# Performance work log

Hardware: AMD Instinct MI355X
Metric: run time of the kernel (lower is better)

The kernel has to match this reference:

```python
import jax, jax.numpy as jnp
import numpy as np

N_HEADS = 8
HEAD_DIM = 64  # hidden_dim 512 / 8 heads
EPS = 1e-12    # F.normalize clamp_min eps


def setup_inputs() -> dict:
    key = jax.random.key(0)
    k1, k2, k3, k4 = jax.random.split(key, 4)
    B, C, H, W = 2, 256, 48, 48
    hidden = N_HEADS * HEAD_DIM
    x = jax.random.normal(k1, (B, C, H, W), dtype=jnp.float32)
    w_qkv = jax.random.normal(k2, (hidden * 3, C), dtype=jnp.float32) * 0.02
    w_proj = jax.random.normal(k3, (C, hidden), dtype=jnp.float32) * 0.02
    b_proj = jax.random.normal(k4, (C,), dtype=jnp.float32) * 0.02
    return {"x": x, "w_qkv": w_qkv, "w_proj": w_proj, "b_proj": b_proj}


def _l2norm_tokens(t):
    # normalize along the token axis (last dim), matching F.normalize(dim=-1)
    n = jnp.sqrt(jnp.sum(t * t, axis=-1, keepdims=True))
    return t / jnp.maximum(n, EPS)


def reference(x, w_qkv, w_proj, b_proj):
    B, C, H, W = x.shape
    N = H * W
    # 1x1 conv == channel matmul
    qkv = jnp.einsum('oc,bchw->bohw', w_qkv, x)  # [B, 3*hidden, H, W]
    qkv = qkv.reshape(B, 3, N_HEADS, HEAD_DIM, N)
    q, k, v = qkv[:, 0], qkv[:, 1], qkv[:, 2]    # each [B, h, d, N]
    q = _l2norm_tokens(q)
    k = _l2norm_tokens(k)
    # attn = q^T @ k over head_dim -> [B, h, N, N]; note: qk_scale unused in source
    attn = jnp.einsum('bhdn,bhdm->bhnm', q, k)
    attn = jax.nn.softmax(attn, axis=-1)
    # out = attn @ v^T -> [B, h, N, d], then permute to [B, h, d, N]
    out = jnp.einsum('bhnm,bhdm->bhdn', attn, v)
    out = out.reshape(B, N_HEADS * HEAD_DIM, H, W)
    # proj 1x1 conv with bias
    y = jnp.einsum('oc,bchw->bohw', w_proj, out) + b_proj[None, :, None, None]
    return y
```

## Files before the change

kernel.cpp:

```cpp
#include <hip/hip_runtime.h>
#include <math.h>

#define NTOK 2304
#define BATCH 2
#define CIN 256
#define HID 512
#define NH 8
#define LOG2E 1.44269504088896340736f

typedef __attribute__((ext_vector_type(8))) short bfrag;
typedef __attribute__((ext_vector_type(16))) float f32x16;

#if __has_builtin(__builtin_amdgcn_exp2f)
#define EXP2(x) __builtin_amdgcn_exp2f(x)
#else
#define EXP2(x) exp2f(x)
#endif

__device__ __forceinline__ unsigned f2bf(float f) {
    unsigned u = __float_as_uint(f);
    u += 0x7FFF + ((u >> 16) & 1);
    return u >> 16;
}

__device__ __forceinline__ float bf2f(unsigned short s) {
    return __uint_as_float(((unsigned)s) << 16);
}

__device__ __forceinline__ unsigned pk_trunc(float a, float b) {
    return __builtin_amdgcn_perm(__float_as_uint(b), __float_as_uint(a), 0x07060302u);
}

__device__ __forceinline__ void softmax_frag(
    const f32x16& accS, int h, float& ps0, float& ps1, bfrag& P0, bfrag& P1)
{
    unsigned dw[8];
    float e0[8], e1[8];
#pragma unroll
    for (int i = 0; i < 8; i++) {
        float plo = EXP2(accS[2 * i]);
        float phi = EXP2(accS[2 * i + 1]);
        dw[i] = pk_trunc(plo, phi);
        e0[i] = __uint_as_float(dw[i] << 16);
        e1[i] = __uint_as_float(dw[i] & 0xffff0000u);
    }
    ps0 += ((e0[0] + e0[1]) + (e0[2] + e0[3])) + ((e0[4] + e0[5]) + (e0[6] + e0[7]));
    ps1 += ((e1[0] + e1[1]) + (e1[2] + e1[3])) + ((e1[4] + e1[5]) + (e1[6] + e1[7]));
    unsigned sa0 = h ? dw[0] : dw[2], sb0 = h ? dw[1] : dw[3];
    unsigned sa1 = h ? dw[4] : dw[6], sb1 = h ? dw[5] : dw[7];
    unsigned ra0 = (unsigned)__shfl_xor((int)sa0, 32, 64);
    unsigned rb0 = (unsigned)__shfl_xor((int)sb0, 32, 64);
    unsigned ra1 = (unsigned)__shfl_xor((int)sa1, 32, 64);
    unsigned rb1 = (unsigned)__shfl_xor((int)sb1, 32, 64);
    union { bfrag f; unsigned u[4]; } U0, U1;
    U0.u[0] = h ? ra0 : dw[0];  U0.u[1] = h ? rb0 : dw[1];
    U0.u[2] = h ? dw[2] : ra0;  U0.u[3] = h ? dw[3] : rb0;
    U1.u[0] = h ? ra1 : dw[4];  U1.u[1] = h ? rb1 : dw[5];
    U1.u[2] = h ? dw[6] : ra1;  U1.u[3] = h ? dw[7] : rb1;
    P0 = U0.f; P1 = U1.f;
}

__global__ __launch_bounds__(256) void pack_all(
    const float* __restrict__ wq, short* __restrict__ wqb,
    const float* __restrict__ wp, short* __restrict__ wpb,
    const float* __restrict__ x, short* __restrict__ xT,
    float* __restrict__ sumsq)
{
    int bid = blockIdx.x;
    if (bid < 288) {
        int n0 = (bid % 36) * 64, c0 = ((bid / 36) & 3) * 64, b = bid / 144;
        __shared__ float sT[64][65];
        int tid = threadIdx.x, lane = tid & 63, wv = tid >> 6;
        for (int c = wv; c < 64; c += 4)
            sT[c][lane] = x[((size_t)b * CIN + c0 + c) * NTOK + n0 + lane];
        __syncthreads();
        int n = tid >> 2, c4 = (tid & 3) * 16;
        unsigned buf[8];
#pragma unroll
        for (int i = 0; i < 8; i++)
            buf[i] = f2bf(sT[c4 + 2 * i][n]) | (f2bf(sT[c4 + 2 * i + 1][n]) << 16);
        int n_tok = n0 + n;
        int l31n = n & 31;
        short* dst = xT + (((size_t)b * 72 + (n_tok >> 5)) * 16 + ((c0 + c4) >> 4)) * 512;
        ((uint4*)(dst + (0 * 32 + l31n) * 8))[0] = make_uint4(buf[0], buf[1], buf[2], buf[3]);
        ((uint4*)(dst + (1 * 32 + l31n) * 8))[0] = make_uint4(buf[4], buf[5], buf[6], buf[7]);
    } else {
        if (bid == 288) {
            ((float4*)sumsq)[threadIdx.x * 2] = make_float4(0.f, 0.f, 0.f, 0.f);
            ((float4*)sumsq)[threadIdx.x * 2 + 1] = make_float4(0.f, 0.f, 0.f, 0.f);
        }
        int e = ((bid - 288) * 256 + threadIdx.x) * 8;
        const int NQ = 1536 * 256;
        const float* src; short* dst;
        if (e < NQ) {
            int row = e >> 8, c = e & 255;
            int off = (((row >> 5) * 16 + (c >> 4)) * 64 + ((c >> 3) & 1) * 32 + (row & 31)) * 8;
            src = wq + e; dst = wqb + off;
        } else {
            int e2 = e - NQ;
            int row = e2 >> 9, c = e2 & 511;
            int off = (((row >> 5) * 32 + (c >> 4)) * 64 + ((c >> 3) & 1) * 32 + (row & 31)) * 8;
            src = wp + e2; dst = wpb + off;
        }
        float4 v0 = ((const float4*)src)[0];
        float4 v1 = ((const float4*)src)[1];
        unsigned b0 = f2bf(v0.x) | (f2bf(v0.y) << 16);
        unsigned b1 = f2bf(v0.z) | (f2bf(v0.w) << 16);
        unsigned b2 = f2bf(v1.x) | (f2bf(v1.y) << 16);
        unsigned b3 = f2bf(v1.z) | (f2bf(v1.w) << 16);
        *((uint4*)dst) = make_uint4(b0, b1, b2, b3);
    }
}

__global__ __launch_bounds__(256, 2) void gemm_qkv(
    const short* __restrict__ A,
    const short* __restrict__ B,
    short* __restrict__ qku,
    short* __restrict__ vb)
{
    int b = blockIdx.z;
    int o0 = blockIdx.y * 128;
    int n0 = blockIdx.x * 128;
    int tid = threadIdx.x, wv = tid >> 6, lane = tid & 63;
    int h = lane >> 5, l31 = lane & 31;

    const short* pa = A + ((size_t)(o0 >> 5) * 16) * 512 + lane * 8;
    const short* pb = B + (((size_t)b * 72 + (n0 >> 5) + wv) * 16) * 512 + lane * 8;

    f32x16 acc[4];
#pragma unroll
    for (int rb = 0; rb < 4; rb++)
#pragma unroll
        for (int r = 0; r < 16; r++) acc[rb][r] = 0.f;

#pragma unroll 2
    for (int kc = 0; kc < 16; kc++) {
        bfrag a0 = *(const bfrag*)(pa + (size_t)(0 * 16 + kc) * 512);
        bfrag a1 = *(const bfrag*)(pa + (size_t)(1 * 16 + kc) * 512);
        bfrag a2 = *(const bfrag*)(pa + (size_t)(2 * 16 + kc) * 512);
        bfrag a3 = *(const bfrag*)(pa + (size_t)(3 * 16 + kc) * 512);
        bfrag bb = *(const bfrag*)(pb + (size_t)kc * 512);
        acc[0] = __builtin_amdgcn_mfma_f32_32x32x16_bf16(a0, bb, acc[0], 0, 0, 0);
        acc[1] = __builtin_amdgcn_mfma_f32_32x32x16_bf16(a1, bb, acc[1], 0, 0, 0);
        acc[2] = __builtin_amdgcn_mfma_f32_32x32x16_bf16(a2, bb, acc[2], 0, 0, 0);
        acc[3] = __builtin_amdgcn_mfma_f32_32x32x16_bf16(a3, bb, acc[3], 0, 0, 0);
    }

    int nn = n0 + wv * 32 + l31;
    if (o0 < 1024) {
        int sel = o0 >> 9;
        short* Qb = qku + (size_t)sel * (16 * NTOK * 64);
        int oo = o0 & 511;
        int tl = nn & 31;
        size_t base_mb = (size_t)(nn >> 5) * 4;
#pragma unroll
        for (int rb = 0; rb < 4; rb++) {
            int hh2 = (oo + rb * 32) >> 6;
            int ihi = (rb & 1) * 2;
            short* Qbb = Qb + (size_t)(b * 8 + hh2) * (NTOK * 64);
#pragma unroll
            for (int q = 0; q < 4; q++) {
                int i = ihi + (q >> 1);
                unsigned lo = f2bf(acc[rb][4 * q])     | (f2bf(acc[rb][4 * q + 1]) << 16);
                unsigned hi = f2bf(acc[rb][4 * q + 2]) | (f2bf(acc[rb][4 * q + 3]) << 16);
                *(uint2*)(Qbb + (base_mb + i) * 512 + ((q & 1) * 32 + tl) * 8 + 4 * h)
                    = make_uint2(lo, hi);
            }
        }
    } else {
        short* V = vb + (size_t)b * 512 * NTOK;
        int ov = o0 - 1024;
        int mb = nn >> 5, jc = (nn >> 4) & 1, hv = (nn >> 3) & 1, e = nn & 7;
#pragma unroll
        for (int rb = 0; rb < 4; rb++)
#pragma unroll
            for (int r = 0; r < 16; r++) {
                int ml = (r & 3) + 8 * (r >> 2) + 4 * h;
                int row = ov + rb * 32 + ml;
                int hh2 = row >> 6, dl = row & 63;
                int jr = dl >> 5, l31v = dl & 31;
                V[((((size_t)hh2 * 72 + mb) * 4 + jr * 2 + jc) * 64
                   + hv * 32 + l31v) * 8 + e] = (short)f2bf(acc[rb][r]);
            }
    }
}

__global__ __launch_bounds__(64) void sumsq_qk(
    const short* __restrict__ qkt, float* __restrict__ sumsq)
{
    int bid = blockIdx.x;
    int mc = bid % 9;
    int rest = bid / 9;
    int i = rest & 3;
    int selbh = rest >> 2;
    int lane = threadIdx.x;
    const short* p = qkt + (((size_t)selbh * 72 + mc * 8) * 4 + i) * 512 + lane * 8;
    float sq[8] = {0.f, 0.f, 0.f, 0.f, 0.f, 0.f, 0.f, 0.f};
#pragma unroll
    for (int m = 0; m < 8; m++) {
        bfrag v = *(const bfrag*)(p + (size_t)m * 2048);
#pragma unroll
        for (int e = 0; e < 8; e++) {
            float f = bf2f((unsigned short)v[e]);
            sq[e] += f * f;
        }
    }
#pragma unroll
    for (int off = 1; off <= 16; off <<= 1)
#pragma unroll
        for (int e = 0; e < 8; e++)
            sq[e] += __shfl_xor(sq[e], off, 64);
    if ((lane & 31) == 0) {
        int sel = selbh >> 4, bh = selbh & 15;
        int b = bh >> 3, hh = bh & 7, hsel = lane >> 5;
        int dbase = i * 16 + hsel * 8;
        float* dst = sumsq + b * 1024 + sel * 512 + hh * 64 + dbase;
#pragma unroll
        for (int e = 0; e < 8; e++) atomicAdd(dst + e, sq[e]);
    }
}

__global__ __launch_bounds__(256) void scale_q(
    short* __restrict__ qkt, const float* __restrict__ sumsq)
{
    int s = blockIdx.x * 256 + threadIdx.x;
    int lane = s & 63;
    int rest = s >> 6;
    int fi = rest & 3;
    int bh = rest / 288;
    int b = bh >> 3, hh = bh & 7;
    int d0 = fi * 16 + (lane >> 5) * 8;
    const float* sq = sumsq + b * 1024 + hh * 64 + d0;
    const float* sk = sumsq + b * 1024 + 512 + hh * 64 + d0;
    float4 q0 = ((const float4*)sq)[0], q1 = ((const float4*)sq)[1];
    float4 k0 = ((const float4*)sk)[0], k1 = ((const float4*)sk)[1];
    float i0 = LOG2E / (fmaxf(sqrtf(q0.x), 1e-12f) * fmaxf(sqrtf(k0.x), 1e-12f));
    float i1 = LOG2E / (fmaxf(sqrtf(q0.y), 1e-12f) * fmaxf(sqrtf(k0.y), 1e-12f));
    float i2 = LOG2E / (fmaxf(sqrtf(q0.z), 1e-12f) * fmaxf(sqrtf(k0.z), 1e-12f));
    float i3 = LOG2E / (fmaxf(sqrtf(q0.w), 1e-12f) * fmaxf(sqrtf(k0.w), 1e-12f));
    float i4 = LOG2E / (fmaxf(sqrtf(q1.x), 1e-12f) * fmaxf(sqrtf(k1.x), 1e-12f));
    float i5 = LOG2E / (fmaxf(sqrtf(q1.y), 1e-12f) * fmaxf(sqrtf(k1.y), 1e-12f));
    float i6 = LOG2E / (fmaxf(sqrtf(q1.z), 1e-12f) * fmaxf(sqrtf(k1.z), 1e-12f));
    float i7 = LOG2E / (fmaxf(sqrtf(q1.w), 1e-12f) * fmaxf(sqrtf(k1.w), 1e-12f));
    uint4 v = ((uint4*)qkt)[s];
    unsigned o0w = f2bf(__uint_as_float(v.x << 16) * i0)
                 | (f2bf(__uint_as_float(v.x & 0xffff0000u) * i1) << 16);
    unsigned o1w = f2bf(__uint_as_float(v.y << 16) * i2)
                 | (f2bf(__uint_as_float(v.y & 0xffff0000u) * i3) << 16);
    unsigned o2w = f2bf(__uint_as_float(v.z << 16) * i4)
                 | (f2bf(__uint_as_float(v.z & 0xffff0000u) * i5) << 16);
    unsigned o3w = f2bf(__uint_as_float(v.w << 16) * i6)
                 | (f2bf(__uint_as_float(v.w & 0xffff0000u) * i7) << 16);
    ((uint4*)qkt)[s] = make_uint4(o0w, o1w, o2w, o3w);
}

__global__ __launch_bounds__(64, 4) void attn_nb(
    const short* __restrict__ qkt,
    const short* __restrict__ vb,
    short* __restrict__ Opart,
    float* __restrict__ lsum)
{
    int bid = blockIdx.x;
    int x = bid & 7;
    int r = bid >> 3;
    int g = x * 8 + r / 72;
    int nbi = r % 72;
    int bh = g >> 2, ms = g & 3;
    int b = bh >> 3, hh = bh & 7;
    int lane = threadIdx.x;
    int h = lane >> 5, l31 = lane & 31;
    int nb = nbi * 32;
    int mb0 = ms * 18;

    const short* Qt = qkt + (size_t)bh * NTOK * 64;
    const short* kp = qkt + (size_t)16 * NTOK * 64 + (size_t)bh * NTOK * 64
                    + ((size_t)mb0 * 4) * 512 + lane * 8;
    const short* vp = vb + (((size_t)(b * 8 + hh) * 72 + mb0) * 4) * 512 + lane * 8;

    bfrag bQ[4];
    {
        const short* q0 = Qt + ((size_t)nbi * 4) * 512 + lane * 8;
#pragma unroll
        for (int i = 0; i < 4; i++) bQ[i] = *(const bfrag*)(q0 + i * 512);
    }

    f32x16 aL, aH;
#pragma unroll
    for (int r2 = 0; r2 < 16; r2++) { aL[r2] = 0.f; aH[r2] = 0.f; }
    float s0 = 0.f, s1 = 0.f;

    bfrag ck[4], cv[4];
#pragma unroll
    for (int i = 0; i < 4; i++) {
        ck[i] = *(const bfrag*)(kp + i * 512);
        cv[i] = *(const bfrag*)(vp + i * 512);
    }

#pragma unroll 2
    for (int it = 0; it < 18; it++) {
        kp += 2048; vp += 2048;
        bfrag nk[4], nv[4];
#pragma unroll
        for (int i = 0; i < 4; i++) {
            nk[i] = *(const bfrag*)(kp + i * 512);
            nv[i] = *(const bfrag*)(vp + i * 512);
        }

        bfrag P0, P1;
        {
            f32x16 accS;
#pragma unroll
            for (int r2 = 0; r2 < 16; r2++) accS[r2] = 0.f;
            accS = __builtin_amdgcn_mfma_f32_32x32x16_bf16(ck[0], bQ[0], accS, 0, 0, 0);
            accS = __builtin_amdgcn_mfma_f32_32x32x16_bf16(ck[1], bQ[1], accS, 0, 0, 0);
            accS = __builtin_amdgcn_mfma_f32_32x32x16_bf16(ck[2], bQ[2], accS, 0, 0, 0);
            accS = __builtin_amdgcn_mfma_f32_32x32x16_bf16(ck[3], bQ[3], accS, 0, 0, 0);
            softmax_frag(accS, h, s0, s1, P0, P1);
        }
        aL = __builtin_amdgcn_mfma_f32_32x32x16_bf16(P0, cv[0], aL, 0, 0, 0);
        aL = __builtin_amdgcn_mfma_f32_32x32x16_bf16(P1, cv[1], aL, 0, 0, 0);
        aH = __builtin_amdgcn_mfma_f32_32x32x16_bf16(P0, cv[2], aH, 0, 0, 0);
        aH = __builtin_amdgcn_mfma_f32_32x32x16_bf16(P1, cv[3], aH, 0, 0, 0);

#pragma unroll
        for (int i = 0; i < 4; i++) { ck[i] = nk[i]; cv[i] = nv[i]; }
    }

    float p0 = s0 + s1;
    p0 += __shfl_xor(p0, 32, 64);
    if (h == 0)
        lsum[((size_t)ms * 16 + bh) * NTOK + nb + l31] = p0;

    short* Ob = Opart + ((size_t)ms * 2 + b) * (72 * 32 * 64 * 8);
    int kcL = hh * 4 + (l31 >> 4);
    int kcH = kcL + 2;
    int e = l31 & 7;
    int hs8 = ((l31 >> 3) & 1) * 32;
#pragma unroll
    for (int r2 = 0; r2 < 16; r2++) {
        int ml = (r2 & 3) + 8 * (r2 >> 2) + 4 * h;
        int wi = hs8 + ml;
        Ob[(((size_t)nbi * 32 + kcL) * 64 + wi) * 8 + e] = (short)f2bf(aL[r2]);
        Ob[(((size_t)nbi * 32 + kcH) * 64 + wi) * 8 + e] = (short)f2bf(aH[r2]);
    }
}

__global__ __launch_bounds__(256) void combine(
    const short* __restrict__ Opart, const float* __restrict__ lsum,
    short* __restrict__ aoT)
{
    int s = blockIdx.x * 256 + threadIdx.x;
    int lane = s & 63, kc = (s >> 6) & 31, nbb = s >> 11;
    int b = nbb >= 72 ? 1 : 0, nb = nbb - 72 * b;
    int l31 = lane & 31;
    int n = nb * 32 + l31;
    int hh = kc >> 2;
    float l = 0.f;
#pragma unroll
    for (int ms = 0; ms < 4; ms++)
        l += lsum[((size_t)ms * 16 + b * 8 + hh) * NTOK + n];
    float inv = 1.f / l;
    const size_t MS = 2ull * 72 * 32 * 64 * 8;
    float a[8] = {0.f, 0.f, 0.f, 0.f, 0.f, 0.f, 0.f, 0.f};
#pragma unroll
    for (int ms = 0; ms < 4; ms++) {
        uint4 v = *(const uint4*)(Opart + (size_t)ms * MS + (size_t)s * 8);
        a[0] += __uint_as_float(v.x << 16);
        a[1] += __uint_as_float(v.x & 0xffff0000u);
        a[2] += __uint_as_float(v.y << 16);
        a[3] += __uint_as_float(v.y & 0xffff0000u);
        a[4] += __uint_as_float(v.z << 16);
        a[5] += __uint_as_float(v.z & 0xffff0000u);
        a[6] += __uint_as_float(v.w << 16);
        a[7] += __uint_as_float(v.w & 0xffff0000u);
    }
    unsigned b0 = f2bf(a[0] * inv) | (f2bf(a[1] * inv) << 16);
    unsigned b1 = f2bf(a[2] * inv) | (f2bf(a[3] * inv) << 16);
    unsigned b2 = f2bf(a[4] * inv) | (f2bf(a[5] * inv) << 16);
    unsigned b3 = f2bf(a[6] * inv) | (f2bf(a[7] * inv) << 16);
    *((uint4*)(aoT + (size_t)s * 8)) = make_uint4(b0, b1, b2, b3);
}

__global__ __launch_bounds__(256, 2) void gemm_proj(
    const short* __restrict__ A,
    const short* __restrict__ B,
    const float* __restrict__ bias, float* __restrict__ y)
{
    int b = blockIdx.z;
    int o0 = blockIdx.y * 64;
    int n0 = blockIdx.x * 128;
    int tid = threadIdx.x, wv = tid >> 6, lane = tid & 63;
    int h = lane >> 5, l31 = lane & 31;

    const short* pa = A + ((size_t)(o0 >> 5) * 32) * 512 + lane * 8;
    const short* pb = B + (((size_t)b * 72 + (n0 >> 5) + wv) * 32) * 512 + lane * 8;

    f32x16 acc0, acc1;
#pragma unroll
    for (int r = 0; r < 16; r++) { acc0[r] = 0.f; acc1[r] = 0.f; }

#pragma unroll 4
    for (int kc = 0; kc < 32; kc++) {
        bfrag a0 = *(const bfrag*)(pa + (size_t)kc * 512);
        bfrag a1 = *(const bfrag*)(pa + (size_t)(32 + kc) * 512);
        bfrag bb = *(const bfrag*)(pb + (size_t)kc * 512);
        acc0 = __builtin_amdgcn_mfma_f32_32x32x16_bf16(a0, bb, acc0, 0, 0, 0);
        acc1 = __builtin_amdgcn_mfma_f32_32x32x16_bf16(a1, bb, acc1, 0, 0, 0);
    }

    int nn = n0 + wv * 32 + l31;
#pragma unroll
    for (int r = 0; r < 16; r++) {
        int ml = (r & 3) + 8 * (r >> 2) + 4 * h;
        y[((size_t)b * CIN + o0 + ml) * NTOK + nn] = acc0[r] + bias[o0 + ml];
        y[((size_t)b * CIN + o0 + 32 + ml) * NTOK + nn] = acc1[r] + bias[o0 + 32 + ml];
    }
}

extern "C" void kernel_launch(void* const* d_in, const int* in_sizes, int n_in,
                              void* d_out, int out_size, void* d_ws, size_t ws_size,
                              hipStream_t stream)
{
    const float* x      = (const float*)d_in[0];
    const float* w_qkv  = (const float*)d_in[1];
    const float* w_proj = (const float*)d_in[2];
    const float* b_proj = (const float*)d_in[3];
    float* y = (float*)d_out;

    short* Opart = (short*)d_ws;
    short* vb    = (short*)((char*)d_ws + 18874368);
    short* qkt   = (short*)((char*)d_ws + 23592960);
    short* aoT   = (short*)((char*)d_ws + 23592960);
    float* lsum  = (float*)((char*)d_ws + 33030144);
    short* xT    = (short*)((char*)d_ws + 33030144);
    short* wqb   = (short*)((char*)d_ws + 35389440);
    short* wpb   = (short*)((char*)d_ws + 36175872);
    float* sumsq = (float*)((char*)d_ws + 36438016);

    pack_all<<<544, 256, 0, stream>>>(w_qkv, wqb, w_proj, wpb, x, xT, sumsq);
    gemm_qkv<<<dim3(NTOK / 128, 1536 / 128, BATCH), 256, 0, stream>>>(
        wqb, xT, qkt, vb);
    sumsq_qk<<<1152, 64, 0, stream>>>(qkt, sumsq);
    scale_q<<<1152, 256, 0, stream>>>(qkt, sumsq);
    attn_nb<<<4608, 64, 0, stream>>>(qkt, vb, Opart, lsum);
    combine<<<1152, 256, 0, stream>>>(Opart, lsum, aoT);
    gemm_proj<<<dim3(NTOK / 128, CIN / 64, BATCH), 256, 0, stream>>>(
        wpb, aoT, b_proj, y);
}
```

Before: 141.9 us.

## Fuse Q scaling into attention and split-combine into projection GEMM

Removes the standalone scale_q kernel by applying the per-dimension normalization scale to Q fragments as they are loaded in attn_nb. Removes the combine kernel by having gemm_proj read the four split partial outputs and lsum directly, sum and normalize them, and feed the result to MFMA. This cuts two launches and a round trip of intermediate buffers through global memory. In exchange, gemm_proj now uses single-wave blocks and reads four times more B data per block, repeated for each of the four output-channel blocks. bf2f must already exist in the hidden code.

```diff
diff --git a/kernel.cpp b/kernel.cpp
--- a/kernel.cpp
+++ b/kernel.cpp
@@ -220,43 +220,10 @@
     }
 }
 
-__global__ __launch_bounds__(256) void scale_q(
-    short* __restrict__ qkt, const float* __restrict__ sumsq)
-{
-    int s = blockIdx.x * 256 + threadIdx.x;
-    int lane = s & 63;
-    int rest = s >> 6;
-    int fi = rest & 3;
-    int bh = rest / 288;
-    int b = bh >> 3, hh = bh & 7;
-    int d0 = fi * 16 + (lane >> 5) * 8;
-    const float* sq = sumsq + b * 1024 + hh * 64 + d0;
-    const float* sk = sumsq + b * 1024 + 512 + hh * 64 + d0;
-    float4 q0 = ((const float4*)sq)[0], q1 = ((const float4*)sq)[1];
-    float4 k0 = ((const float4*)sk)[0], k1 = ((const float4*)sk)[1];
-    float i0 = LOG2E / (fmaxf(sqrtf(q0.x), 1e-12f) * fmaxf(sqrtf(k0.x), 1e-12f));
-    float i1 = LOG2E / (fmaxf(sqrtf(q0.y), 1e-12f) * fmaxf(sqrtf(k0.y), 1e-12f));
-    float i2 = LOG2E / (fmaxf(sqrtf(q0.z), 1e-12f) * fmaxf(sqrtf(k0.z), 1e-12f));
-    float i3 = LOG2E / (fmaxf(sqrtf(q0.w), 1e-12f) * fmaxf(sqrtf(k0.w), 1e-12f));
-    float i4 = LOG2E / (fmaxf(sqrtf(q1.x), 1e-12f) * fmaxf(sqrtf(k1.x), 1e-12f));
-    float i5 = LOG2E / (fmaxf(sqrtf(q1.y), 1e-12f) * fmaxf(sqrtf(k1.y), 1e-12f));
-    float i6 = LOG2E / (fmaxf(sqrtf(q1.z), 1e-12f) * fmaxf(sqrtf(k1.z), 1e-12f));
-    float i7 = LOG2E / (fmaxf(sqrtf(q1.w), 1e-12f) * fmaxf(sqrtf(k1.w), 1e-12f));
-    uint4 v = ((uint4*)qkt)[s];
-    unsigned o0w = f2bf(__uint_as_float(v.x << 16) * i0)
-                 | (f2bf(__uint_as_float(v.x & 0xffff0000u) * i1) << 16);
-    unsigned o1w = f2bf(__uint_as_float(v.y << 16) * i2)
-                 | (f2bf(__uint_as_float(v.y & 0xffff0000u) * i3) << 16);
-    unsigned o2w = f2bf(__uint_as_float(v.z << 16) * i4)
-                 | (f2bf(__uint_as_float(v.z & 0xffff0000u) * i5) << 16);
-    unsigned o3w = f2bf(__uint_as_float(v.w << 16) * i6)
-                 | (f2bf(__uint_as_float(v.w & 0xffff0000u) * i7) << 16);
-    ((uint4*)qkt)[s] = make_uint4(o0w, o1w, o2w, o3w);
-}
-
 __global__ __launch_bounds__(64, 4) void attn_nb(
     const short* __restrict__ qkt,
     const short* __restrict__ vb,
+    const float* __restrict__ sumsq,
     short* __restrict__ Opart,
     float* __restrict__ lsum)
 {
@@ -280,8 +247,31 @@
     bfrag bQ[4];
     {
         const short* q0 = Qt + ((size_t)nbi * 4) * 512 + lane * 8;
-#pragma unroll
-        for (int i = 0; i < 4; i++) bQ[i] = *(const bfrag*)(q0 + i * 512);
+        const float* sq = sumsq + b * 1024 + hh * 64;
+        const float* sk = sumsq + b * 1024 + 512 + hh * 64;
+#pragma unroll
+        for (int i = 0; i < 4; i++) {
+            bfrag qr = *(const bfrag*)(q0 + i * 512);
+            int d0 = i * 16 + h * 8;
+            float4 a0 = *(const float4*)(sq + d0);
+            float4 a1 = *(const float4*)(sq + d0 + 4);
+            float4 c0 = *(const float4*)(sk + d0);
+            float4 c1 = *(const float4*)(sk + d0 + 4);
+            float iv[8];
+            iv[0] = LOG2E / (fmaxf(sqrtf(a0.x), 1e-12f) * fmaxf(sqrtf(c0.x), 1e-12f));
+            iv[1] = LOG2E / (fmaxf(sqrtf(a0.y), 1e-12f) * fmaxf(sqrtf(c0.y), 1e-12f));
+            iv[2] = LOG2E / (fmaxf(sqrtf(a0.z), 1e-12f) * fmaxf(sqrtf(c0.z), 1e-12f));
+            iv[3] = LOG2E / (fmaxf(sqrtf(a0.w), 1e-12f) * fmaxf(sqrtf(c0.w), 1e-12f));
+            iv[4] = LOG2E / (fmaxf(sqrtf(a1.x), 1e-12f) * fmaxf(sqrtf(c1.x), 1e-12f));
+            iv[5] = LOG2E / (fmaxf(sqrtf(a1.y), 1e-12f) * fmaxf(sqrtf(c1.y), 1e-12f));
+            iv[6] = LOG2E / (fmaxf(sqrtf(a1.z), 1e-12f) * fmaxf(sqrtf(c1.z), 1e-12f));
+            iv[7] = LOG2E / (fmaxf(sqrtf(a1.w), 1e-12f) * fmaxf(sqrtf(c1.w), 1e-12f));
+            union { bfrag f; unsigned short u[8]; } U;
+#pragma unroll
+            for (int e = 0; e < 8; e++)
+                U.u[e] = (unsigned short)f2bf(bf2f((unsigned short)qr[e]) * iv[e]);
+            bQ[i] = U.f;
+        }
     }
 
     f32x16 aL, aH;
@@ -345,70 +335,73 @@
     }
 }
 
-__global__ __launch_bounds__(256) void combine(
-    const short* __restrict__ Opart, const float* __restrict__ lsum,
-    short* __restrict__ aoT)
-{
-    int s = blockIdx.x * 256 + threadIdx.x;
-    int lane = s & 63, kc = (s >> 6) & 31, nbb = s >> 11;
-    int b = nbb >= 72 ? 1 : 0, nb = nbb - 72 * b;
-    int l31 = lane & 31;
-    int n = nb * 32 + l31;
-    int hh = kc >> 2;
-    float l = 0.f;
-#pragma unroll
-    for (int ms = 0; ms < 4; ms++)
-        l += lsum[((size_t)ms * 16 + b * 8 + hh) * NTOK + n];
-    float inv = 1.f / l;
+__global__ __launch_bounds__(64) void gemm_proj(
+    const short* __restrict__ A,
+    const short* __restrict__ Opart,
+    const float* __restrict__ lsum,
+    const float* __restrict__ bias, float* __restrict__ y)
+{
+    int bid = blockIdx.x;
+    int nbi = bid % 72;
+    int rest = bid / 72;
+    int ob = rest & 3, b = rest >> 2;
+    int o0 = ob * 64;
+    int lane = threadIdx.x;
+    int h = lane >> 5, l31 = lane & 31;
+    int n = nbi * 32 + l31;
+
+    const short* pa = A + ((size_t)(o0 >> 5) * 32) * 512 + lane * 8;
+    const short* pB = Opart + (size_t)b * (72 * 32 * 64 * 8)
+                    + ((size_t)nbi * 32) * 512 + lane * 8;
     const size_t MS = 2ull * 72 * 32 * 64 * 8;
-    float a[8] = {0.f, 0.f, 0.f, 0.f, 0.f, 0.f, 0.f, 0.f};
-#pragma unroll
-    for (int ms = 0; ms < 4; ms++) {
-        uint4 v = *(const uint4*)(Opart + (size_t)ms * MS + (size_t)s * 8);
-        a[0] += __uint_as_float(v.x << 16);
-        a[1] += __uint_as_float(v.x & 0xffff0000u);
-        a[2] += __uint_as_float(v.y << 16);
-        a[3] += __uint_as_float(v.y & 0xffff0000u);
-        a[4] += __uint_as_float(v.z << 16);
-        a[5] += __uint_as_float(v.z & 0xffff0000u);
-        a[6] += __uint_as_float(v.w << 16);
-        a[7] += __uint_as_float(v.w & 0xffff0000u);
-    }
-    unsigned b0 = f2bf(a[0] * inv) | (f2bf(a[1] * inv) << 16);
-    unsigned b1 = f2bf(a[2] * inv) | (f2bf(a[3] * inv) << 16);
-    unsigned b2 = f2bf(a[4] * inv) | (f2bf(a[5] * inv) << 16);
-    unsigned b3 = f2bf(a[6] * inv) | (f2bf(a[7] * inv) << 16);
-    *((uint4*)(aoT + (size_t)s * 8)) = make_uint4(b0, b1, b2, b3);
-}
-
-__global__ __launch_bounds__(256, 2) void gemm_proj(
-    const short* __restrict__ A,
-    const short* __restrict__ B,
-    const float* __restrict__ bias, float* __restrict__ y)
-{
-    int b = blockIdx.z;
-    int o0 = blockIdx.y * 64;
-    int n0 = blockIdx.x * 128;
-    int tid = threadIdx.x, wv = tid >> 6, lane = tid & 63;
-    int h = lane >> 5, l31 = lane & 31;
-
-    const short* pa = A + ((size_t)(o0 >> 5) * 32) * 512 + lane * 8;
-    const short* pb = B + (((size_t)b * 72 + (n0 >> 5) + wv) * 32) * 512 + lane * 8;
 
     f32x16 acc0, acc1;
 #pragma unroll
     for (int r = 0; r < 16; r++) { acc0[r] = 0.f; acc1[r] = 0.f; }
 
+    float linv = 0.f;
 #pragma unroll 4
     for (int kc = 0; kc < 32; kc++) {
+        if ((kc & 3) == 0) {
+            int hh = kc >> 2;
+            float lt = lsum[((size_t)0 * 16 + b * 8 + hh) * NTOK + n]
+                     + lsum[((size_t)1 * 16 + b * 8 + hh) * NTOK + n]
+                     + lsum[((size_t)2 * 16 + b * 8 + hh) * NTOK + n]
+                     + lsum[((size_t)3 * 16 + b * 8 + hh) * NTOK + n];
+            linv = 1.f / lt;
+        }
         bfrag a0 = *(const bfrag*)(pa + (size_t)kc * 512);
         bfrag a1 = *(const bfrag*)(pa + (size_t)(32 + kc) * 512);
-        bfrag bb = *(const bfrag*)(pb + (size_t)kc * 512);
-        acc0 = __builtin_amdgcn_mfma_f32_32x32x16_bf16(a0, bb, acc0, 0, 0, 0);
-        acc1 = __builtin_amdgcn_mfma_f32_32x32x16_bf16(a1, bb, acc1, 0, 0, 0);
-    }
-
-    int nn = n0 + wv * 32 + l31;
+        uint4 v0 = *(const uint4*)(pB + 0 * MS + (size_t)kc * 512);
+        uint4 v1 = *(const uint4*)(pB + 1 * MS + (size_t)kc * 512);
+        uint4 v2 = *(const uint4*)(pB + 2 * MS + (size_t)kc * 512);
+        uint4 v3 = *(const uint4*)(pB + 3 * MS + (size_t)kc * 512);
+        float s0 = (__uint_as_float(v0.x << 16) + __uint_as_float(v1.x << 16))
+                 + (__uint_as_float(v2.x << 16) + __uint_as_float(v3.x << 16));
+        float s1 = (__uint_as_float(v0.x & 0xffff0000u) + __uint_as_float(v1.x & 0xffff0000u))
+                 + (__uint_as_float(v2.x & 0xffff0000u) + __uint_as_float(v3.x & 0xffff0000u));
+        float s2 = (__uint_as_float(v0.y << 16) + __uint_as_float(v1.y << 16))
+                 + (__uint_as_float(v2.y << 16) + __uint_as_float(v3.y << 16));
+        float s3 = (__uint_as_float(v0.y & 0xffff0000u) + __uint_as_float(v1.y & 0xffff0000u))
+                 + (__uint_as_float(v2.y & 0xffff0000u) + __uint_as_float(v3.y & 0xffff0000u));
+        float s4 = (__uint_as_float(v0.z << 16) + __uint_as_float(v1.z << 16))
+                 + (__uint_as_float(v2.z << 16) + __uint_as_float(v3.z << 16));
+        float s5 = (__uint_as_float(v0.z & 0xffff0000u) + __uint_as_float(v1.z & 0xffff0000u))
+                 + (__uint_as_float(v2.z & 0xffff0000u) + __uint_as_float(v3.z & 0xffff0000u));
+        float s6 = (__uint_as_float(v0.w << 16) + __uint_as_float(v1.w << 16))
+                 + (__uint_as_float(v2.w << 16) + __uint_as_float(v3.w << 16));
+        float s7 = (__uint_as_float(v0.w & 0xffff0000u) + __uint_as_float(v1.w & 0xffff0000u))
+                 + (__uint_as_float(v2.w & 0xffff0000u) + __uint_as_float(v3.w & 0xffff0000u));
+        union { bfrag f; unsigned u[4]; } B;
+        B.u[0] = f2bf(s0 * linv) | (f2bf(s1 * linv) << 16);
+        B.u[1] = f2bf(s2 * linv) | (f2bf(s3 * linv) << 16);
+        B.u[2] = f2bf(s4 * linv) | (f2bf(s5 * linv) << 16);
+        B.u[3] = f2bf(s6 * linv) | (f2bf(s7 * linv) << 16);
+        acc0 = __builtin_amdgcn_mfma_f32_32x32x16_bf16(a0, B.f, acc0, 0, 0, 0);
+        acc1 = __builtin_amdgcn_mfma_f32_32x32x16_bf16(a1, B.f, acc1, 0, 0, 0);
+    }
+
+    int nn = nbi * 32 + l31;
 #pragma unroll
     for (int r = 0; r < 16; r++) {
         int ml = (r & 3) + 8 * (r >> 2) + 4 * h;
@@ -430,7 +423,6 @@
     short* Opart = (short*)d_ws;
     short* vb    = (short*)((char*)d_ws + 18874368);
     short* qkt   = (short*)((char*)d_ws + 23592960);
-    short* aoT   = (short*)((char*)d_ws + 23592960);
     float* lsum  = (float*)((char*)d_ws + 33030144);
     short* xT    = (short*)((char*)d_ws + 33030144);
     short* wqb   = (short*)((char*)d_ws + 35389440);
@@ -441,9 +433,6 @@
     gemm_qkv<<<dim3(NTOK / 128, 1536 / 128, BATCH), 256, 0, stream>>>(
         wqb, xT, qkt, vb);
     sumsq_qk<<<1152, 64, 0, stream>>>(qkt, sumsq);
-    scale_q<<<1152, 256, 0, stream>>>(qkt, sumsq);
-    attn_nb<<<4608, 64, 0, stream>>>(qkt, vb, Opart, lsum);
-    combine<<<1152, 256, 0, stream>>>(Opart, lsum, aoT);
-    gemm_proj<<<dim3(NTOK / 128, CIN / 64, BATCH), 256, 0, stream>>>(
-        wpb, aoT, b_proj, y);
-}
+    attn_nb<<<4608, 64, 0, stream>>>(qkt, vb, sumsq, Opart, lsum);
+    gemm_proj<<<576, 64, 0, stream>>>(wpb, Opart, lsum, b_proj, y);
+}
```

New measurement: 156.3 us. 10.2% more time.
